# Optimization experiments

Hardware: AMD Instinct MI355X
Metric: run time of the kernel (lower is better)

Reference implementation:

```python
import jax, jax.numpy as jnp
import numpy as np

N_NODES = 50000
N_EDGES = 800000
F_IN = 64
HIDDEN = 64
N_CLASSES = 8
NUM_GRAPHS = 500


def setup_inputs() -> dict:
    key = jax.random.key(0)
    ks = jax.random.split(key, 12)
    x = jax.random.normal(ks[0], (N_NODES, F_IN), dtype=jnp.float32)
    edge_index = jax.random.randint(ks[1], (2, N_EDGES), 0, N_NODES, dtype=jnp.int64)
    batch = jnp.sort(jax.random.randint(ks[2], (N_NODES,), 0, NUM_GRAPHS, dtype=jnp.int64))
    def glorot(k, fan_in, fan_out):
        s = (6.0 / (fan_in + fan_out)) ** 0.5
        return jax.random.uniform(k, (fan_in, fan_out), jnp.float32, -s, s)
    return {
        "x": x,
        "edge_index": edge_index,
        "batch": batch,
        "W1": glorot(ks[3], F_IN, HIDDEN), "b1": jnp.zeros((HIDDEN,), jnp.float32),
        "W2": glorot(ks[4], HIDDEN, HIDDEN), "b2": jnp.zeros((HIDDEN,), jnp.float32),
        "W3": glorot(ks[5], HIDDEN, HIDDEN), "b3": jnp.zeros((HIDDEN,), jnp.float32),
        "Wl": glorot(ks[6], HIDDEN, N_CLASSES), "bl": jnp.zeros((N_CLASSES,), jnp.float32),
    }


def _gcn_conv(x, row, col, norm, W, b, n):
    # GCNConv: linear transform, gather source nodes, scale by sym-norm, scatter-add to targets.
    xw = x @ W                                  # [N, H]
    msg = xw[row] * norm[:, None]               # [E+N, H]
    out = jax.ops.segment_sum(msg, col, num_segments=n)
    return out + b


def reference(x, edge_index, batch, W1, b1, W2, b2, W3, b3, Wl, bl):
    n = x.shape[0]
    loop = jnp.arange(n, dtype=edge_index.dtype)
    row = jnp.concatenate([edge_index[0], loop])  # source nodes (+ self loops)
    col = jnp.concatenate([edge_index[1], loop])  # target nodes (+ self loops)
    deg = jax.ops.segment_sum(jnp.ones_like(col, dtype=x.dtype), col, num_segments=n)
    dinv = jnp.where(deg > 0, jax.lax.rsqrt(deg), 0.0)
    norm = dinv[row] * dinv[col]                # symmetric normalization per edge

    h = jax.nn.relu(_gcn_conv(x, row, col, norm, W1, b1, n))
    h = jax.nn.relu(_gcn_conv(h, row, col, norm, W2, b2, n))
    h = _gcn_conv(h, row, col, norm, W3, b3, n)

    # global mean pool over graphs
    sums = jax.ops.segment_sum(h, batch, num_segments=NUM_GRAPHS)
    cnts = jax.ops.segment_sum(jnp.ones((n,), x.dtype), batch, num_segments=NUM_GRAPHS)
    embed = sums / jnp.maximum(cnts, 1.0)[:, None]

    # dropout p=0.5 is identity in eval mode
    return embed @ Wl + bl
```

## Files before the change

kernel.cpp:

```cpp
#include <hip/hip_runtime.h>
#include <hip/hip_bf16.h>
#include <hip/hip_fp16.h>

#define HID      64
#define N_CLS    8
#define N_GRAPHS 500
#define PAD      64
#define BW       128
#define NB       391
#define CHUNK    4096
#define CAP_BLK  48

__global__ __launch_bounds__(1024) void k_bin_gemm(
        const int* __restrict__ row, const int* __restrict__ col, int E,
        unsigned int* __restrict__ ebuf, unsigned short* __restrict__ cnt_tbl,
        const float* __restrict__ Hx, const float* __restrict__ W1,
        const float* __restrict__ dinv_unused, __half* __restrict__ O, int N) {
    __shared__ float smem[4096];
    int t = threadIdx.x;
    int nEb = (E + CHUNK - 1) / CHUNK;

    if ((int)blockIdx.x < nEb) {
        int* cur = (int*)smem;
        int bi = blockIdx.x;
        for (int i = t; i < NB; i += 1024) cur[i] = 0;
        __syncthreads();
        int e = bi * CHUNK + t * 4;
        if (e < E) {
            int4 c4 = *reinterpret_cast<const int4*>(col + e);
            int4 r4 = *reinterpret_cast<const int4*>(row + e);
            int b0 = c4.x >> 7, b1 = c4.y >> 7, b2 = c4.z >> 7, b3 = c4.w >> 7;
            int s0 = atomicAdd(&cur[b0], 1);
            int s1 = atomicAdd(&cur[b1], 1);
            int s2 = atomicAdd(&cur[b2], 1);
            int s3 = atomicAdd(&cur[b3], 1);
            size_t base = (size_t)bi * NB;
            if (s0 < CAP_BLK) ebuf[(base + b0) * CAP_BLK + s0] = ((unsigned)(c4.x & 127) << 16) | (unsigned)r4.x;
            if (s1 < CAP_BLK) ebuf[(base + b1) * CAP_BLK + s1] = ((unsigned)(c4.y & 127) << 16) | (unsigned)r4.y;
            if (s2 < CAP_BLK) ebuf[(base + b2) * CAP_BLK + s2] = ((unsigned)(c4.z & 127) << 16) | (unsigned)r4.z;
            if (s3 < CAP_BLK) ebuf[(base + b3) * CAP_BLK + s3] = ((unsigned)(c4.w & 127) << 16) | (unsigned)r4.w;
        }
        __syncthreads();
        for (int i = t; i < NB; i += 1024)
            cnt_tbl[(size_t)bi * NB + i] = (unsigned short)min(cur[i], CAP_BLK);
        return;
    }
    int gb = blockIdx.x - nEb;
    float* Ws = smem;
    #pragma unroll
    for (int i = t; i < 64 * 64; i += 1024) Ws[i] = W1[i];
    __syncthreads();
    int c = t & 63;
    float w[64];
    #pragma unroll
    for (int k = 0; k < 64; ++k) w[k] = Ws[k * 64 + c];

    int rbase = gb * 128 + (t >> 6) * 8;
    #pragma unroll 1
    for (int it = 0; it < 8; it += 2) {
        int r0 = rbase + it;
        if (r0 >= N) break;
        int r0u = __builtin_amdgcn_readfirstlane(r0);
        int has1 = (r0u + 1 < N);
        const float* __restrict__ h0 = Hx + (size_t)r0u * HID;
        const float* __restrict__ h1 = Hx + (size_t)(has1 ? r0u + 1 : r0u) * HID;
        float a0 = 0.f, a1 = 0.f, a2 = 0.f, a3 = 0.f;
        float b0 = 0.f, b1 = 0.f, b2 = 0.f, b3 = 0.f;
        #pragma unroll
        for (int k = 0; k < 64; k += 4) {
            a0 = fmaf(h0[k],     w[k],     a0);
            b0 = fmaf(h1[k],     w[k],     b0);
            a1 = fmaf(h0[k + 1], w[k + 1], a1);
            b1 = fmaf(h1[k + 1], w[k + 1], b1);
            a2 = fmaf(h0[k + 2], w[k + 2], a2);
            b2 = fmaf(h1[k + 2], w[k + 2], b2);
            a3 = fmaf(h0[k + 3], w[k + 3], a3);
            b3 = fmaf(h1[k + 3], w[k + 3], b3);
        }
        O[(size_t)r0u * HID + c] = __float2half((a0 + a1) + (a2 + a3));
        if (has1)
            O[(size_t)(r0u + 1) * HID + c] = __float2half((b0 + b1) + (b2 + b3));
    }
}

__global__ __launch_bounds__(512) void k_fill(const unsigned int* __restrict__ ebuf,
                                              const unsigned short* __restrict__ cnt_tbl,
                                              int nEb,
                                              unsigned short* __restrict__ adj,
                                              int* __restrict__ cnt,
                                              float* __restrict__ dinv, int N) {
    int t = threadIdx.x;
    int b = blockIdx.x;
    __shared__ int pfx[256];
    __shared__ int lcnt[BW];
    if (t < BW) lcnt[t] = 0;
    if (t < 256) pfx[t] = (t < nEb) ? (int)cnt_tbl[(size_t)t * NB + b] : 0;
    __syncthreads();
    #pragma unroll
    for (int off = 1; off < 256; off <<= 1) {
        int v = (t < 256 && t >= off) ? pfx[t - off] : 0;
        __syncthreads();
        if (t < 256) pfx[t] += v;
        __syncthreads();
    }
    int m = pfx[nEb - 1];
    for (int g = t; g < m; g += 512) {
        int lo = 0, hi = nEb - 1;
        while (lo < hi) {
            int mid = (lo + hi) >> 1;
            if (pfx[mid] > g) hi = mid; else lo = mid + 1;
        }
        int bi = lo;
        int sl = g - (bi ? pfx[bi - 1] : 0);
        unsigned u = ebuf[((size_t)bi * NB + b) * CAP_BLK + sl];
        int cl = u >> 16;
        int r  = u & 0xFFFF;
        int p = atomicAdd(&lcnt[cl], 1);
        if (p < PAD) adj[((size_t)(b * BW + cl)) * PAD + p] = (unsigned short)r;
    }
    __syncthreads();
    int node = b * BW + t;
    if (t < BW && node < N) {
        int n = lcnt[t];
        cnt[node] = n;
        dinv[node] = rsqrtf((float)n + 1.0f);
    }
}

__global__ __launch_bounds__(256) void k_gemm64(const float* __restrict__ H,
                                                const float* __restrict__ W,
                                                const float* __restrict__ dinv,
                                                __half* __restrict__ O, int N) {
    __shared__ float Ws[64 * 64];
    int tid = threadIdx.x;
    #pragma unroll
    for (int i = tid; i < 64 * 64; i += 256) Ws[i] = W[i];
    __syncthreads();
    int c = tid & 63;
    float w[64];
    #pragma unroll
    for (int k = 0; k < 64; ++k) w[k] = Ws[k * 64 + c];

    int rbase = blockIdx.x * 32 + (tid >> 6) * 8;
    #pragma unroll 1
    for (int it = 0; it < 8; it += 2) {
        int r0 = rbase + it;
        if (r0 >= N) break;
        int r0u = __builtin_amdgcn_readfirstlane(r0);
        int has1 = (r0u + 1 < N);
        const float* __restrict__ h0 = H + (size_t)r0u * HID;
        const float* __restrict__ h1 = H + (size_t)(has1 ? r0u + 1 : r0u) * HID;
        float a0 = 0.f, a1 = 0.f, a2 = 0.f, a3 = 0.f;
        float b0 = 0.f, b1 = 0.f, b2 = 0.f, b3 = 0.f;
        #pragma unroll
        for (int k = 0; k < 64; k += 4) {
            a0 = fmaf(h0[k],     w[k],     a0);
            b0 = fmaf(h1[k],     w[k],     b0);
            a1 = fmaf(h0[k + 1], w[k + 1], a1);
            b1 = fmaf(h1[k + 1], w[k + 1], b1);
            a2 = fmaf(h0[k + 2], w[k + 2], a2);
            b2 = fmaf(h1[k + 2], w[k + 2], b2);
            a3 = fmaf(h0[k + 3], w[k + 3], a3);
            b3 = fmaf(h1[k + 3], w[k + 3], b3);
        }
        O[(size_t)r0u * HID + c] = __float2half(((a0 + a1) + (a2 + a3)) * dinv[r0u]);
        if (has1)
            O[(size_t)(r0u + 1) * HID + c] =
                __float2half(((b0 + b1) + (b2 + b3)) * dinv[r0u + 1]);
    }
}

__global__ __launch_bounds__(256) void k_gather(const unsigned short* __restrict__ adj,
                                                const int* __restrict__ cnt,
                                                const float* __restrict__ dinv,
                                                const __half* __restrict__ xh,
                                                const float* __restrict__ b,
                                                float* __restrict__ out,
                                                int N, int do_relu, int edge_scale) {
    int node = blockIdx.x * 4 + (threadIdx.x >> 6);
    if (node >= N) return;
    int lane = threadIdx.x & 63;
    int o = lane >> 3, j = lane & 7;
    size_t s = (size_t)node * PAD;
    int n = min(cnt[node], PAD);
    float dv = dinv[node];
    int r_all = adj[s + lane];

    float a[8] = {0.f, 0.f, 0.f, 0.f, 0.f, 0.f, 0.f, 0.f};
    for (int base = 0; base < n; base += 16) {
        int i1 = base + o;
        int i2 = base + 8 + o;
        int r1 = __shfl(r_all, i1, 64);
        int r2 = __shfl(r_all, i2, 64);
        if (i1 < n) {
            float sc = edge_scale ? dinv[r1] : 1.0f;
            uint4 u = *reinterpret_cast<const uint4*>(xh + (size_t)r1 * HID + j * 8);
            float2 f0 = __half22float2(*reinterpret_cast<__half2*>(&u.x));
            float2 f1 = __half22float2(*reinterpret_cast<__half2*>(&u.y));
            float2 f2 = __half22float2(*reinterpret_cast<__half2*>(&u.z));
            float2 f3 = __half22float2(*reinterpret_cast<__half2*>(&u.w));
            a[0] = fmaf(f0.x, sc, a[0]); a[1] = fmaf(f0.y, sc, a[1]);
            a[2] = fmaf(f1.x, sc, a[2]); a[3] = fmaf(f1.y, sc, a[3]);
            a[4] = fmaf(f2.x, sc, a[4]); a[5] = fmaf(f2.y, sc, a[5]);
            a[6] = fmaf(f3.x, sc, a[6]); a[7] = fmaf(f3.y, sc, a[7]);
        }
        if (i2 < n) {
            float sc = edge_scale ? dinv[r2] : 1.0f;
            uint4 u = *reinterpret_cast<const uint4*>(xh + (size_t)r2 * HID + j * 8);
            float2 f0 = __half22float2(*reinterpret_cast<__half2*>(&u.x));
            float2 f1 = __half22float2(*reinterpret_cast<__half2*>(&u.y));
            float2 f2 = __half22float2(*reinterpret_cast<__half2*>(&u.z));
            float2 f3 = __half22float2(*reinterpret_cast<__half2*>(&u.w));
            a[0] = fmaf(f0.x, sc, a[0]); a[1] = fmaf(f0.y, sc, a[1]);
            a[2] = fmaf(f1.x, sc, a[2]); a[3] = fmaf(f1.y, sc, a[3]);
            a[4] = fmaf(f2.x, sc, a[4]); a[5] = fmaf(f2.y, sc, a[5]);
            a[6] = fmaf(f3.x, sc, a[6]); a[7] = fmaf(f3.y, sc, a[7]);
        }
    }
    if (o == 0) {
        float sc = edge_scale ? dv : 1.0f;
        uint4 u = *reinterpret_cast<const uint4*>(xh + (size_t)node * HID + j * 8);
        float2 f0 = __half22float2(*reinterpret_cast<__half2*>(&u.x));
        float2 f1 = __half22float2(*reinterpret_cast<__half2*>(&u.y));
        float2 f2 = __half22float2(*reinterpret_cast<__half2*>(&u.z));
        float2 f3 = __half22float2(*reinterpret_cast<__half2*>(&u.w));
        a[0] = fmaf(f0.x, sc, a[0]); a[1] = fmaf(f0.y, sc, a[1]);
        a[2] = fmaf(f1.x, sc, a[2]); a[3] = fmaf(f1.y, sc, a[3]);
        a[4] = fmaf(f2.x, sc, a[4]); a[5] = fmaf(f2.y, sc, a[5]);
        a[6] = fmaf(f3.x, sc, a[6]); a[7] = fmaf(f3.y, sc, a[7]);
    }
    #pragma unroll
    for (int k = 0; k < 8; ++k) {
        a[k] += __shfl_xor(a[k], 8, 64);
        a[k] += __shfl_xor(a[k], 16, 64);
        a[k] += __shfl_xor(a[k], 32, 64);
    }
    if (o == 0) {
        const float4 b0 = *reinterpret_cast<const float4*>(b + j * 8);
        const float4 b1 = *reinterpret_cast<const float4*>(b + j * 8 + 4);
        float4 o0, o1;
        o0.x = a[0] * dv + b0.x; o0.y = a[1] * dv + b0.y;
        o0.z = a[2] * dv + b0.z; o0.w = a[3] * dv + b0.w;
        o1.x = a[4] * dv + b1.x; o1.y = a[5] * dv + b1.y;
        o1.z = a[6] * dv + b1.z; o1.w = a[7] * dv + b1.w;
        if (do_relu) {
            o0.x = fmaxf(o0.x, 0.f); o0.y = fmaxf(o0.y, 0.f);
            o0.z = fmaxf(o0.z, 0.f); o0.w = fmaxf(o0.w, 0.f);
            o1.x = fmaxf(o1.x, 0.f); o1.y = fmaxf(o1.y, 0.f);
            o1.z = fmaxf(o1.z, 0.f); o1.w = fmaxf(o1.w, 0.f);
        }
        *reinterpret_cast<float4*>(out + (size_t)node * HID + j * 8)     = o0;
        *reinterpret_cast<float4*>(out + (size_t)node * HID + j * 8 + 4) = o1;
    }
}

__global__ __launch_bounds__(256) void k_fgh2(const unsigned short* __restrict__ adj,
                                              const int* __restrict__ cnt,
                                              const float* __restrict__ dinv,
                                              const __half* __restrict__ xh,
                                              const float* __restrict__ b,
                                              const float* __restrict__ Wl,
                                              float* __restrict__ y,
                                              int N) {
    int node = blockIdx.x * 4 + (threadIdx.x >> 6);
    if (node >= N) return;
    int lane = threadIdx.x & 63;
    int o = lane >> 3, j = lane & 7;
    size_t s = (size_t)node * PAD;
    int n = min(cnt[node], PAD);
    float dv = dinv[node];
    int r_all = adj[s + lane];

    float a[8] = {0.f, 0.f, 0.f, 0.f, 0.f, 0.f, 0.f, 0.f};
    for (int base = 0; base < n; base += 16) {
        int i1 = base + o;
        int i2 = base + 8 + o;
        int r1 = __shfl(r_all, i1, 64);
        int r2 = __shfl(r_all, i2, 64);
        if (i1 < n) {
            uint4 u = *reinterpret_cast<const uint4*>(xh + (size_t)r1 * HID + j * 8);
            float2 f0 = __half22float2(*reinterpret_cast<__half2*>(&u.x));
            float2 f1 = __half22float2(*reinterpret_cast<__half2*>(&u.y));
            float2 f2 = __half22float2(*reinterpret_cast<__half2*>(&u.z));
            float2 f3 = __half22float2(*reinterpret_cast<__half2*>(&u.w));
            a[0] += f0.x; a[1] += f0.y; a[2] += f1.x; a[3] += f1.y;
            a[4] += f2.x; a[5] += f2.y; a[6] += f3.x; a[7] += f3.y;
        }
        if (i2 < n) {
            uint4 u = *reinterpret_cast<const uint4*>(xh + (size_t)r2 * HID + j * 8);
            float2 f0 = __half22float2(*reinterpret_cast<__half2*>(&u.x));
            float2 f1 = __half22float2(*reinterpret_cast<__half2*>(&u.y));
            float2 f2 = __half22float2(*reinterpret_cast<__half2*>(&u.z));
            float2 f3 = __half22float2(*reinterpret_cast<__half2*>(&u.w));
            a[0] += f0.x; a[1] += f0.y; a[2] += f1.x; a[3] += f1.y;
            a[4] += f2.x; a[5] += f2.y; a[6] += f3.x; a[7] += f3.y;
        }
    }
    if (o == 0) {
        uint4 u = *reinterpret_cast<const uint4*>(xh + (size_t)node * HID + j * 8);
        float2 f0 = __half22float2(*reinterpret_cast<__half2*>(&u.x));
        float2 f1 = __half22float2(*reinterpret_cast<__half2*>(&u.y));
        float2 f2 = __half22float2(*reinterpret_cast<__half2*>(&u.z));
        float2 f3 = __half22float2(*reinterpret_cast<__half2*>(&u.w));
        a[0] += f0.x; a[1] += f0.y; a[2] += f1.x; a[3] += f1.y;
        a[4] += f2.x; a[5] += f2.y; a[6] += f3.x; a[7] += f3.y;
    }
    #pragma unroll
    for (int k = 0; k < 8; ++k) {
        a[k] += __shfl_xor(a[k], 8, 64);
        a[k] += __shfl_xor(a[k], 16, 64);
        a[k] += __shfl_xor(a[k], 32, 64);
    }
    const float4 bv0 = *reinterpret_cast<const float4*>(b + j * 8);
    const float4 bv1 = *reinterpret_cast<const float4*>(b + j * 8 + 4);
    float h[8];
    h[0] = fmaf(a[0], dv, bv0.x); h[1] = fmaf(a[1], dv, bv0.y);
    h[2] = fmaf(a[2], dv, bv0.z); h[3] = fmaf(a[3], dv, bv0.w);
    h[4] = fmaf(a[4], dv, bv1.x); h[5] = fmaf(a[5], dv, bv1.y);
    h[6] = fmaf(a[6], dv, bv1.z); h[7] = fmaf(a[7], dv, bv1.w);
    float p = 0.f;
    #pragma unroll
    for (int m = 0; m < 8; ++m)
        p = fmaf(h[m], Wl[(j * 8 + m) * N_CLS + o], p);
    p += __shfl_xor(p, 1, 64);
    p += __shfl_xor(p, 2, 64);
    p += __shfl_xor(p, 4, 64);
    if (j == 0) y[(size_t)node * N_CLS + o] = p;
}

__global__ __launch_bounds__(256) void k_pmean8(const float* __restrict__ y,
                                                const int* __restrict__ batch, int N,
                                                const float* __restrict__ bl,
                                                float* __restrict__ out) {
    int g = blockIdx.x;
    int t = threadIdx.x;
    int lo = 0, hi = N;
    while (lo < hi) { int mid = (lo + hi) >> 1; if (batch[mid] < g) lo = mid + 1; else hi = mid; }
    int s = lo;
    int lo2 = s, hi2 = N;
    while (lo2 < hi2) { int mid = (lo2 + hi2) >> 1; if (batch[mid] < g + 1) lo2 = mid + 1; else hi2 = mid; }
    int n = lo2 - s;

    int c = t & 7, idx = t >> 3;
    float acc = 0.f;
    for (int i = s + idx; i < s + n; i += 32) acc += y[(size_t)i * N_CLS + c];
    __shared__ float lds[256];
    lds[t] = acc;
    __syncthreads();
    for (int s2 = 16; s2 > 0; s2 >>= 1) {
        if (idx < s2) lds[t] += lds[t + s2 * 8];
        __syncthreads();
    }
    if (t < N_CLS)
        out[(size_t)g * N_CLS + t] = lds[t] / fmaxf((float)n, 1.0f) + bl[t];
}

extern "C" void kernel_launch(void* const* d_in, const int* in_sizes, int n_in,
                              void* d_out, int out_size, void* d_ws, size_t ws_size,
                              hipStream_t stream) {
    const float* x     = (const float*)d_in[0];
    const int*   ei    = (const int*)d_in[1];
    const int*   batch = (const int*)d_in[2];
    const float* W1    = (const float*)d_in[3];
    const float* b1    = (const float*)d_in[4];
    const float* W2    = (const float*)d_in[5];
    const float* b2    = (const float*)d_in[6];
    const float* W3    = (const float*)d_in[7];
    const float* b3    = (const float*)d_in[8];
    const float* Wl    = (const float*)d_in[9];
    const float* bl    = (const float*)d_in[10];
    float* out = (float*)d_out;

    const int N = in_sizes[0] / HID;
    const int E = in_sizes[1] / 2;
    const int* row = ei;
    const int* col = ei + E;

    const int nEb = (E + CHUNK - 1) / CHUNK;

    char* wsb = (char*)d_ws;
    int*   cnt  = (int*)wsb;
    float* dinv = (float*)(cnt + 50048);
    unsigned short* cnt_tbl = (unsigned short*)(dinv + 50048);
    unsigned int*   ebuf    = (unsigned int*)((int*)cnt_tbl + 40000);
    unsigned short* adj     = (unsigned short*)(ebuf + (size_t)nEb * NB * CAP_BLK);
    __half* bufH = (__half*)(adj + (size_t)50048 * PAD);
    float*  bufB = (float*)(bufH + (size_t)50048 * HID);
    float*  ybuf = bufB + (size_t)50048 * HID;

    const int T = 256;
    const int gGemmF = (N + 127) / 128;
    const int gGemm  = (N + 31) / 32;
    const int gGath  = (N + 3) / 4;

    k_bin_gemm<<<nEb + gGemmF, 1024, 0, stream>>>(row, col, E, ebuf, cnt_tbl,
                                                  x, W1, nullptr, bufH, N);
    k_fill<<<NB, 512, 0, stream>>>(ebuf, cnt_tbl, nEb, adj, cnt, dinv, N);

    k_gather<<<gGath, T, 0, stream>>>(adj, cnt, dinv, bufH, b1, bufB, N, 1, 1);
    k_gemm64<<<gGemm, T, 0, stream>>>(bufB, W2, dinv, bufH, N);
    k_gather<<<gGath, T, 0, stream>>>(adj, cnt, dinv, bufH, b2, bufB, N, 1, 0);
    k_gemm64<<<gGemm, T, 0, stream>>>(bufB, W3, dinv, bufH, N);
    k_fgh2<<<gGath, T, 0, stream>>>(adj, cnt, dinv, bufH, b3, Wl, ybuf, N);

    k_pmean8<<<N_GRAPHS, T, 0, stream>>>(ybuf, batch, N, bl, out);
}
```

Baseline: 181.6 us.

## Fuse neighbor gather with next-layer 64x64 GEMM into one kernel

Merges the aggregation kernel and the following dense 64x64 transform into one kernel, k_gg. Each wavefront aggregates a node's neighbors, applies bias and ReLU, then multiplies by W held in shared memory, using lane shuffles to broadcast the hidden vector. The result is written directly as fp16 pre-scaled by dinv. This removes the fp32 intermediate round-trip through global memory and two kernel launches per layer. In exchange, every 4-node block reloads the 16KB weight matrix into LDS and all lanes now do the dot-product work.

```diff
diff --git a/kernel.cpp b/kernel.cpp
--- a/kernel.cpp
+++ b/kernel.cpp
@@ -15,7 +15,7 @@
         const int* __restrict__ row, const int* __restrict__ col, int E,
         unsigned int* __restrict__ ebuf, unsigned short* __restrict__ cnt_tbl,
         const float* __restrict__ Hx, const float* __restrict__ W1,
-        const float* __restrict__ dinv_unused, __half* __restrict__ O, int N) {
+        __half* __restrict__ O, int N) {
     __shared__ float smem[4096];
     int t = threadIdx.x;
     int nEb = (E + CHUNK - 1) / CHUNK;
@@ -127,59 +127,23 @@
     }
 }
 
-__global__ __launch_bounds__(256) void k_gemm64(const float* __restrict__ H,
-                                                const float* __restrict__ W,
-                                                const float* __restrict__ dinv,
-                                                __half* __restrict__ O, int N) {
+__global__ __launch_bounds__(256) void k_gg(const unsigned short* __restrict__ adj,
+                                            const int* __restrict__ cnt,
+                                            const float* __restrict__ dinv,
+                                            const __half* __restrict__ xh,
+                                            const float* __restrict__ b,
+                                            const float* __restrict__ W,
+                                            __half* __restrict__ xh_out,
+                                            int N, int edge_scale) {
     __shared__ float Ws[64 * 64];
-    int tid = threadIdx.x;
-    #pragma unroll
-    for (int i = tid; i < 64 * 64; i += 256) Ws[i] = W[i];
-    __syncthreads();
-    int c = tid & 63;
-    float w[64];
-    #pragma unroll
-    for (int k = 0; k < 64; ++k) w[k] = Ws[k * 64 + c];
-
-    int rbase = blockIdx.x * 32 + (tid >> 6) * 8;
-    #pragma unroll 1
-    for (int it = 0; it < 8; it += 2) {
-        int r0 = rbase + it;
-        if (r0 >= N) break;
-        int r0u = __builtin_amdgcn_readfirstlane(r0);
-        int has1 = (r0u + 1 < N);
-        const float* __restrict__ h0 = H + (size_t)r0u * HID;
-        const float* __restrict__ h1 = H + (size_t)(has1 ? r0u + 1 : r0u) * HID;
-        float a0 = 0.f, a1 = 0.f, a2 = 0.f, a3 = 0.f;
-        float b0 = 0.f, b1 = 0.f, b2 = 0.f, b3 = 0.f;
-        #pragma unroll
-        for (int k = 0; k < 64; k += 4) {
-            a0 = fmaf(h0[k],     w[k],     a0);
-            b0 = fmaf(h1[k],     w[k],     b0);
-            a1 = fmaf(h0[k + 1], w[k + 1], a1);
-            b1 = fmaf(h1[k + 1], w[k + 1], b1);
-            a2 = fmaf(h0[k + 2], w[k + 2], a2);
-            b2 = fmaf(h1[k + 2], w[k + 2], b2);
-            a3 = fmaf(h0[k + 3], w[k + 3], a3);
-            b3 = fmaf(h1[k + 3], w[k + 3], b3);
-        }
-        O[(size_t)r0u * HID + c] = __float2half(((a0 + a1) + (a2 + a3)) * dinv[r0u]);
-        if (has1)
-            O[(size_t)(r0u + 1) * HID + c] =
-                __float2half(((b0 + b1) + (b2 + b3)) * dinv[r0u + 1]);
-    }
-}
-
-__global__ __launch_bounds__(256) void k_gather(const unsigned short* __restrict__ adj,
-                                                const int* __restrict__ cnt,
-                                                const float* __restrict__ dinv,
-                                                const __half* __restrict__ xh,
-                                                const float* __restrict__ b,
-                                                float* __restrict__ out,
-                                                int N, int do_relu, int edge_scale) {
-    int node = blockIdx.x * 4 + (threadIdx.x >> 6);
+    int t = threadIdx.x;
+    #pragma unroll
+    for (int i = t; i < 64 * 64; i += 256) Ws[i] = W[i];
+    __syncthreads();
+
+    int node = blockIdx.x * 4 + (t >> 6);
     if (node >= N) return;
-    int lane = threadIdx.x & 63;
+    int lane = t & 63;
     int o = lane >> 3, j = lane & 7;
     size_t s = (size_t)node * PAD;
     int n = min(cnt[node], PAD);
@@ -217,17 +181,19 @@
             a[6] = fmaf(f3.x, sc, a[6]); a[7] = fmaf(f3.y, sc, a[7]);
         }
     }
-    if (o == 0) {
+    {
         float sc = edge_scale ? dv : 1.0f;
-        uint4 u = *reinterpret_cast<const uint4*>(xh + (size_t)node * HID + j * 8);
-        float2 f0 = __half22float2(*reinterpret_cast<__half2*>(&u.x));
-        float2 f1 = __half22float2(*reinterpret_cast<__half2*>(&u.y));
-        float2 f2 = __half22float2(*reinterpret_cast<__half2*>(&u.z));
-        float2 f3 = __half22float2(*reinterpret_cast<__half2*>(&u.w));
-        a[0] = fmaf(f0.x, sc, a[0]); a[1] = fmaf(f0.y, sc, a[1]);
-        a[2] = fmaf(f1.x, sc, a[2]); a[3] = fmaf(f1.y, sc, a[3]);
-        a[4] = fmaf(f2.x, sc, a[4]); a[5] = fmaf(f2.y, sc, a[5]);
-        a[6] = fmaf(f3.x, sc, a[6]); a[7] = fmaf(f3.y, sc, a[7]);
+        if (o == 0) {
+            uint4 u = *reinterpret_cast<const uint4*>(xh + (size_t)node * HID + j * 8);
+            float2 f0 = __half22float2(*reinterpret_cast<__half2*>(&u.x));
+            float2 f1 = __half22float2(*reinterpret_cast<__half2*>(&u.y));
+            float2 f2 = __half22float2(*reinterpret_cast<__half2*>(&u.z));
+            float2 f3 = __half22float2(*reinterpret_cast<__half2*>(&u.w));
+            a[0] = fmaf(f0.x, sc, a[0]); a[1] = fmaf(f0.y, sc, a[1]);
+            a[2] = fmaf(f1.x, sc, a[2]); a[3] = fmaf(f1.y, sc, a[3]);
+            a[4] = fmaf(f2.x, sc, a[4]); a[5] = fmaf(f2.y, sc, a[5]);
+            a[6] = fmaf(f3.x, sc, a[6]); a[7] = fmaf(f3.y, sc, a[7]);
+        }
     }
     #pragma unroll
     for (int k = 0; k < 8; ++k) {
@@ -235,23 +201,24 @@
         a[k] += __shfl_xor(a[k], 16, 64);
         a[k] += __shfl_xor(a[k], 32, 64);
     }
-    if (o == 0) {
-        const float4 b0 = *reinterpret_cast<const float4*>(b + j * 8);
-        const float4 b1 = *reinterpret_cast<const float4*>(b + j * 8 + 4);
-        float4 o0, o1;
-        o0.x = a[0] * dv + b0.x; o0.y = a[1] * dv + b0.y;
-        o0.z = a[2] * dv + b0.z; o0.w = a[3] * dv + b0.w;
-        o1.x = a[4] * dv + b1.x; o1.y = a[5] * dv + b1.y;
-        o1.z = a[6] * dv + b1.z; o1.w = a[7] * dv + b1.w;
-        if (do_relu) {
-            o0.x = fmaxf(o0.x, 0.f); o0.y = fmaxf(o0.y, 0.f);
-            o0.z = fmaxf(o0.z, 0.f); o0.w = fmaxf(o0.w, 0.f);
-            o1.x = fmaxf(o1.x, 0.f); o1.y = fmaxf(o1.y, 0.f);
-            o1.z = fmaxf(o1.z, 0.f); o1.w = fmaxf(o1.w, 0.f);
-        }
-        *reinterpret_cast<float4*>(out + (size_t)node * HID + j * 8)     = o0;
-        *reinterpret_cast<float4*>(out + (size_t)node * HID + j * 8 + 4) = o1;
-    }
+    const float4 bv0 = *reinterpret_cast<const float4*>(b + j * 8);
+    const float4 bv1 = *reinterpret_cast<const float4*>(b + j * 8 + 4);
+    float h[8];
+    h[0] = fmaxf(fmaf(a[0], dv, bv0.x), 0.f);
+    h[1] = fmaxf(fmaf(a[1], dv, bv0.y), 0.f);
+    h[2] = fmaxf(fmaf(a[2], dv, bv0.z), 0.f);
+    h[3] = fmaxf(fmaf(a[3], dv, bv0.w), 0.f);
+    h[4] = fmaxf(fmaf(a[4], dv, bv1.x), 0.f);
+    h[5] = fmaxf(fmaf(a[5], dv, bv1.y), 0.f);
+    h[6] = fmaxf(fmaf(a[6], dv, bv1.z), 0.f);
+    h[7] = fmaxf(fmaf(a[7], dv, bv1.w), 0.f);
+    float acc = 0.f;
+    #pragma unroll
+    for (int k = 0; k < 64; ++k) {
+        float hk = __shfl(h[k & 7], k >> 3, 64);
+        acc = fmaf(hk, Ws[k * 64 + lane], acc);
+    }
+    xh_out[(size_t)node * HID + lane] = __float2half(acc * dv);
 }
 
 __global__ __launch_bounds__(256) void k_fgh2(const unsigned short* __restrict__ adj,
@@ -384,24 +351,21 @@
     unsigned short* cnt_tbl = (unsigned short*)(dinv + 50048);
     unsigned int*   ebuf    = (unsigned int*)((int*)cnt_tbl + 40000);
     unsigned short* adj     = (unsigned short*)(ebuf + (size_t)nEb * NB * CAP_BLK);
-    __half* bufH = (__half*)(adj + (size_t)50048 * PAD);
-    float*  bufB = (float*)(bufH + (size_t)50048 * HID);
-    float*  ybuf = bufB + (size_t)50048 * HID;
+    __half* bufH1 = (__half*)(adj + (size_t)50048 * PAD);
+    __half* bufH2 = bufH1 + (size_t)50048 * HID;
+    float*  ybuf  = (float*)(bufH2 + (size_t)50048 * HID);
 
     const int T = 256;
     const int gGemmF = (N + 127) / 128;
-    const int gGemm  = (N + 31) / 32;
     const int gGath  = (N + 3) / 4;
 
     k_bin_gemm<<<nEb + gGemmF, 1024, 0, stream>>>(row, col, E, ebuf, cnt_tbl,
-                                                  x, W1, nullptr, bufH, N);
+                                                  x, W1, bufH1, N);
     k_fill<<<NB, 512, 0, stream>>>(ebuf, cnt_tbl, nEb, adj, cnt, dinv, N);
 
-    k_gather<<<gGath, T, 0, stream>>>(adj, cnt, dinv, bufH, b1, bufB, N, 1, 1);
-    k_gemm64<<<gGemm, T, 0, stream>>>(bufB, W2, dinv, bufH, N);
-    k_gather<<<gGath, T, 0, stream>>>(adj, cnt, dinv, bufH, b2, bufB, N, 1, 0);
-    k_gemm64<<<gGemm, T, 0, stream>>>(bufB, W3, dinv, bufH, N);
-    k_fgh2<<<gGath, T, 0, stream>>>(adj, cnt, dinv, bufH, b3, Wl, ybuf, N);
+    k_gg<<<gGath, T, 0, stream>>>(adj, cnt, dinv, bufH1, b1, W2, bufH2, N, 1);
+    k_gg<<<gGath, T, 0, stream>>>(adj, cnt, dinv, bufH2, b2, W3, bufH1, N, 0);
+    k_fgh2<<<gGath, T, 0, stream>>>(adj, cnt, dinv, bufH1, b3, Wl, ybuf, N);
 
     k_pmean8<<<N_GRAPHS, T, 0, stream>>>(ybuf, batch, N, bl, out);
 }
```

Measured after the change: 223.4 us. +23.0%, slower.
